# Performance work log

Hardware: AMD Instinct MI355X
Metric: run time of the kernel (lower is better)

## Reference

```python
import jax, jax.numpy as jnp
import numpy as np

D_MODEL = 1024
NUM_HEADS = 16
D_K = D_MODEL // NUM_HEADS
B, T = 2, 2048


def setup_inputs() -> dict:
    key = jax.random.key(0)
    ks = jax.random.split(key, 9)
    s = 1.0 / np.sqrt(D_MODEL)
    inp = {"x": jax.random.normal(ks[0], (B, T, D_MODEL), dtype=jnp.float32)}
    for i, name in enumerate(["q", "k", "v", "out"]):
        inp[f"W_{name}"] = jax.random.uniform(ks[1 + 2 * i], (D_MODEL, D_MODEL), jnp.float32, -s, s)
        inp[f"b_{name}"] = jax.random.uniform(ks[2 + 2 * i], (D_MODEL,), jnp.float32, -s, s)
    return inp


def reference(x, W_q, b_q, W_k, b_k, W_v, b_v, W_out, b_out):
    b, t, _ = x.shape
    # torch Linear: y = x @ W.T + b
    def proj(inp, W, bias):
        y = inp @ W.T + bias
        return y.reshape(b, -1, NUM_HEADS, D_K).transpose(0, 2, 1, 3)  # [B,H,T,d_k]

    Q = proj(x, W_q, b_q)
    K = proj(x, W_k, b_k)
    V = proj(x, W_v, b_v)
    scores = jnp.einsum("bhqd,bhkd->bhqk", Q, K) / jnp.sqrt(jnp.float32(D_K))
    attn = jax.nn.softmax(scores, axis=-1)
    ctx = jnp.einsum("bhqk,bhkd->bhqd", attn, V)
    ctx = ctx.transpose(0, 2, 1, 3).reshape(b, t, D_MODEL)
    return ctx @ W_out.T + b_out
```

## Files before the change

### kernel.cpp

```cpp
#include <hip/hip_runtime.h>
#include <hip/hip_bf16.h>

typedef __attribute__((ext_vector_type(8))) short short8;
typedef __attribute__((ext_vector_type(4))) short short4v;
typedef __attribute__((ext_vector_type(4))) float floatx4;

__device__ __forceinline__ unsigned short f2b(float f) {
  unsigned int v;
  __builtin_memcpy(&v, &f, 4);
  unsigned int r = (v + 0x7FFFu + ((v >> 16) & 1u)) >> 16;
  return (unsigned short)r;
}

__device__ __forceinline__ unsigned int f2b_pk(float a, float b) {
  unsigned int ua, ub;
  __builtin_memcpy(&ua, &a, 4);
  __builtin_memcpy(&ub, &b, 4);
  ua = ua + 0x7FFFu + ((ua >> 16) & 1u);
  ub = ub + 0x7FFFu + ((ub >> 16) & 1u);
#if __has_builtin(__builtin_amdgcn_perm)
  return __builtin_amdgcn_perm(ub, ua, 0x07060302u);
#else
  return (ub & 0xFFFF0000u) | (ua >> 16);
#endif
}

__device__ __forceinline__ float fast_exp2(float x) {
#if __has_builtin(__builtin_amdgcn_exp2f)
  return __builtin_amdgcn_exp2f(x);
#else
  return __builtin_exp2f(x);
#endif
}

__device__ __forceinline__ void async_copy16(const void* g, void* l) {
  __builtin_amdgcn_global_load_lds(
      (const __attribute__((address_space(1))) unsigned int*)g,
      (__attribute__((address_space(3))) unsigned int*)l, 16, 0, 0);
}

#define QSCALE 0.18033688011112042f

__global__ __launch_bounds__(256) void cvt_all_kernel(
    const float* __restrict__ x,
    const float* __restrict__ w0, const float* __restrict__ w1,
    const float* __restrict__ w2, const float* __restrict__ w3,
    unsigned short* __restrict__ xb,
    unsigned short* __restrict__ d0, unsigned short* __restrict__ d1,
    unsigned short* __restrict__ d2, unsigned short* __restrict__ d3)
{
  int gid = blockIdx.x * 256 + threadIdx.x;
  const float* src;
  unsigned short* dst;
  size_t off;
  if (gid < (1 << 20)) {
    src = x; dst = xb; off = gid;
  } else {
    int g = gid - (1 << 20);
    int w = g >> 18;
    off = g & 0x3FFFF;
    src = (w == 0) ? w0 : (w == 1) ? w1 : (w == 2) ? w2 : w3;
    dst = (w == 0) ? d0 : (w == 1) ? d1 : (w == 2) ? d2 : d3;
  }
  floatx4 v = *(const floatx4*)(src + off * 4);
  unsigned int lo = f2b_pk(v[0], v[1]), hi = f2b_pk(v[2], v[3]);
  unsigned long long r = ((unsigned long long)hi << 32) | lo;
  *(unsigned long long*)(dst + off * 4) = r;
}

__global__ __launch_bounds__(256) void gemm_qkv_kernel(
    const unsigned short* __restrict__ A,
    const unsigned short* __restrict__ W0, const unsigned short* __restrict__ W1,
    const unsigned short* __restrict__ W2,
    const float* __restrict__ bias0, const float* __restrict__ bias1,
    const float* __restrict__ bias2,
    unsigned short* __restrict__ Qo, unsigned short* __restrict__ Ko,
    unsigned short* __restrict__ VTo)
{
  const int z = blockIdx.z;
  const unsigned short* W  = (z == 0) ? W0 : (z == 1) ? W1 : W2;
  const float* bias        = (z == 0) ? bias0 : (z == 1) ? bias1 : bias2;

  __shared__ alignas(16) unsigned short sA[128 * 64];
  __shared__ alignas(16) unsigned short sB[128 * 64];

  const int tid  = threadIdx.x;
  const int lane = tid & 63;
  const int wave = tid >> 6;
  const int col  = lane & 15;
  const int quad = lane >> 4;
  const int wm   = (wave >> 1) * 64;
  const int wn   = (wave & 1) * 64;
  const int m0   = blockIdx.y * 128;
  const int n0   = blockIdx.x * 128;
  const int c7   = col & 7;

  floatx4 acc[4][4];
#pragma unroll
  for (int i = 0; i < 4; ++i)
#pragma unroll
    for (int j = 0; j < 4; ++j) acc[i][j] = (floatx4){0.f, 0.f, 0.f, 0.f};

  for (int k0 = 0; k0 < 1024; k0 += 64) {
    __syncthreads();
#pragma unroll
    for (int i = 0; i < 4; ++i) {
      int c   = i * 256 + tid;
      int row = c >> 3;
      int ko  = ((c & 7) ^ (row & 7)) * 8;
      async_copy16(A + (size_t)(m0 + row) * 1024 + k0 + ko, sA + c * 8);
      async_copy16(W + (size_t)(n0 + row) * 1024 + k0 + ko, sB + c * 8);
    }
    __syncthreads();
#pragma unroll
    for (int ks = 0; ks < 2; ++ks) {
      const int rp = ((ks * 4 + quad) ^ c7) * 8;
      short8 af[4], bf[4];
#pragma unroll
      for (int mi = 0; mi < 4; ++mi)
        af[mi] = *(const short8*)(sA + (wm + mi * 16 + col) * 64 + rp);
#pragma unroll
      for (int ni = 0; ni < 4; ++ni)
        bf[ni] = *(const short8*)(sB + (wn + ni * 16 + col) * 64 + rp);
#pragma unroll
      for (int mi = 0; mi < 4; ++mi)
#pragma unroll
        for (int ni = 0; ni < 4; ++ni)
          acc[mi][ni] = __builtin_amdgcn_mfma_f32_16x16x32_bf16(af[mi], bf[ni], acc[mi][ni], 0, 0, 0);
    }
  }

#pragma unroll
  for (int ni = 0; ni < 4; ++ni) {
    int n = n0 + wn + ni * 16 + col;
    float bv = bias[n];
#pragma unroll
    for (int mi = 0; mi < 4; ++mi) {
      int mbase = m0 + wm + mi * 16 + quad * 4;
      if (z == 2) {
        int d = n & 63, h = n >> 6;
        int bb = mbase >> 11, t = mbase & 2047;
        unsigned int lo = f2b_pk(acc[mi][ni][0] + bv, acc[mi][ni][1] + bv);
        unsigned int hi = f2b_pk(acc[mi][ni][2] + bv, acc[mi][ni][3] + bv);
        unsigned long long wv = ((unsigned long long)hi << 32) | lo;
        *(unsigned long long*)(VTo + (((size_t)bb * 16 + h) * 64 + d) * 2048 + t) = wv;
      } else {
#pragma unroll
        for (int r = 0; r < 4; ++r) {
          int m = mbase + r;
          float val = acc[mi][ni][r] + bv;
          if (z == 0) Qo[(size_t)m * 1024 + n] = f2b(val * QSCALE);
          else        Ko[(size_t)m * 1024 + n] = f2b(val);
        }
      }
    }
  }
}

__global__ __launch_bounds__(256) void gemm_out_kernel(
    const unsigned short* __restrict__ A, const unsigned short* __restrict__ W,
    const float* __restrict__ bias, float* __restrict__ DF)
{
  __shared__ alignas(16) unsigned short sA[128 * 64];
  __shared__ alignas(16) unsigned short sB[128 * 64];

  const int tid  = threadIdx.x;
  const int lane = tid & 63;
  const int wave = tid >> 6;
  const int col  = lane & 15;
  const int quad = lane >> 4;
  const int wm   = (wave >> 1) * 64;
  const int wn   = (wave & 1) * 64;
  const int m0   = blockIdx.y * 128;
  const int n0   = blockIdx.x * 128;
  const int c7   = col & 7;

  floatx4 acc[4][4];
#pragma unroll
  for (int i = 0; i < 4; ++i)
#pragma unroll
    for (int j = 0; j < 4; ++j) acc[i][j] = (floatx4){0.f, 0.f, 0.f, 0.f};

  for (int k0 = 0; k0 < 1024; k0 += 64) {
    __syncthreads();
#pragma unroll
    for (int i = 0; i < 4; ++i) {
      int c   = i * 256 + tid;
      int row = c >> 3;
      int ko  = ((c & 7) ^ (row & 7)) * 8;
      async_copy16(A + (size_t)(m0 + row) * 1024 + k0 + ko, sA + c * 8);
      async_copy16(W + (size_t)(n0 + row) * 1024 + k0 + ko, sB + c * 8);
    }
    __syncthreads();
#pragma unroll
    for (int ks = 0; ks < 2; ++ks) {
      const int rp = ((ks * 4 + quad) ^ c7) * 8;
      short8 af[4], bf[4];
#pragma unroll
      for (int mi = 0; mi < 4; ++mi)
        af[mi] = *(const short8*)(sA + (wm + mi * 16 + col) * 64 + rp);
#pragma unroll
      for (int ni = 0; ni < 4; ++ni)
        bf[ni] = *(const short8*)(sB + (wn + ni * 16 + col) * 64 + rp);
#pragma unroll
      for (int mi = 0; mi < 4; ++mi)
#pragma unroll
        for (int ni = 0; ni < 4; ++ni)
          acc[mi][ni] = __builtin_amdgcn_mfma_f32_16x16x32_bf16(af[mi], bf[ni], acc[mi][ni], 0, 0, 0);
    }
  }

#pragma unroll
  for (int ni = 0; ni < 4; ++ni) {
    int n = n0 + wn + ni * 16 + col;
    float bv = bias[n];
#pragma unroll
    for (int mi = 0; mi < 4; ++mi) {
      int mbase = m0 + wm + mi * 16 + quad * 4;
#pragma unroll
      for (int r = 0; r < 4; ++r)
        DF[(size_t)(mbase + r) * 1024 + n] = acc[mi][ni][r] + bv;
    }
  }
}

__global__ __launch_bounds__(256, 2) void attention_kernel(
    const unsigned short* __restrict__ Q, const unsigned short* __restrict__ K,
    const unsigned short* __restrict__ VT, unsigned short* __restrict__ CTX)
{
  __shared__ alignas(16) unsigned short sK[2][4096];
  __shared__ alignas(16) unsigned short sV[2][4096];
  __shared__ alignas(16) unsigned short sP[4][32 * 64];

  const int flat = blockIdx.x;
  const int idx  = flat >> 3;
  const int bh   = (flat & 7) * 4 + (idx >> 4);
  const int q0   = (idx & 15) * 128;
  const int b = bh >> 4, h = bh & 15;

  const int tid  = threadIdx.x;
  const int lane = tid & 63;
  const int wave = tid >> 6;
  const int col  = lane & 15;
  const int quad = lane >> 4;
  const int c7   = col & 7;
  const int swz8 = (quad ^ ((col >> 1) & 3)) * 8;

  const int srow = tid >> 2;
  const int sko  = ((tid & 3) ^ ((tid >> 3) & 3)) * 8;

  const unsigned short* kbase = K + ((size_t)b * 2048 + srow) * 1024 + h * 64;
  const unsigned short* vbase = VT + ((size_t)bh * 64 + srow) * 2048;

  short8 qfA[2], qfB[2];
  {
    const unsigned short* qp =
        Q + ((size_t)(b * 2048 + q0 + wave * 32 + col)) * 1024 + h * 64 + quad * 8;
    qfA[0] = *(const short8*)qp;
    qfA[1] = *(const short8*)(qp + 32);
    qfB[0] = *(const short8*)(qp + 16 * 1024);
    qfB[1] = *(const short8*)(qp + 16 * 1024 + 32);
  }

#pragma unroll
  for (int i = 0; i < 2; ++i) {
    async_copy16(kbase + i * 32 + sko, sK[0] + (i * 256 + tid) * 8);
    async_copy16(vbase + i * 32 + sko, sV[0] + (i * 256 + tid) * 8);
  }

  floatx4 OA[4], OB[4];
#pragma unroll
  for (int f = 0; f < 4; ++f) {
    OA[f] = (floatx4){0.f, 0.f, 0.f, 0.f};
    OB[f] = (floatx4){0.f, 0.f, 0.f, 0.f};
  }
  float laccA = 0.f, laccB = 0.f;

  unsigned short* myP = &sP[wave][0];

#pragma unroll 2
  for (int kt = 0; kt < 2048; kt += 64) {
    const int cur = (kt >> 6) & 1;
    const unsigned short* sKc = sK[cur];
    const unsigned short* sVc = sV[cur];
    __syncthreads();
    if (kt + 64 < 2048) {
      const int nxt = cur ^ 1;
#pragma unroll
      for (int i = 0; i < 2; ++i) {
        async_copy16(kbase + (size_t)(kt + 64) * 1024 + i * 32 + sko,
                     sK[nxt] + (i * 256 + tid) * 8);
        async_copy16(vbase + (kt + 64) + i * 32 + sko,
                     sV[nxt] + (i * 256 + tid) * 8);
      }
    }

    floatx4 STA[4], STB[4];
    __builtin_amdgcn_s_setprio(1);
#pragma unroll
    for (int f = 0; f < 4; ++f) {
      short8 kf0 = *(const short8*)(sKc + (f * 16 + col) * 32 + swz8);
      short8 kf1 = *(const short8*)(sKc + 2048 + (f * 16 + col) * 32 + swz8);
      STA[f] = (floatx4){0.f, 0.f, 0.f, 0.f};
      STA[f] = __builtin_amdgcn_mfma_f32_16x16x32_bf16(kf0, qfA[0], STA[f], 0, 0, 0);
      STA[f] = __builtin_amdgcn_mfma_f32_16x16x32_bf16(kf1, qfA[1], STA[f], 0, 0, 0);
      STB[f] = (floatx4){0.f, 0.f, 0.f, 0.f};
      STB[f] = __builtin_amdgcn_mfma_f32_16x16x32_bf16(kf0, qfB[0], STB[f], 0, 0, 0);
      STB[f] = __builtin_amdgcn_mfma_f32_16x16x32_bf16(kf1, qfB[1], STB[f], 0, 0, 0);
    }
    __builtin_amdgcn_s_setprio(0);

#pragma unroll
    for (int f = 0; f < 4; ++f) {
      float a0 = fast_exp2(STA[f][0]);
      float a1 = fast_exp2(STA[f][1]);
      float a2 = fast_exp2(STA[f][2]);
      float a3 = fast_exp2(STA[f][3]);
      laccA += (a0 + a1) + (a2 + a3);
      unsigned long long wA =
          ((unsigned long long)f2b_pk(a2, a3) << 32) | f2b_pk(a0, a1);
      *(unsigned long long*)(myP + col * 64 +
                             (((f * 2 + (quad >> 1)) ^ c7) * 8) + (quad & 1) * 4) = wA;
      float b0 = fast_exp2(STB[f][0]);
      float b1 = fast_exp2(STB[f][1]);
      float b2 = fast_exp2(STB[f][2]);
      float b3 = fast_exp2(STB[f][3]);
      laccB += (b0 + b1) + (b2 + b3);
      unsigned long long wB =
          ((unsigned long long)f2b_pk(b2, b3) << 32) | f2b_pk(b0, b1);
      *(unsigned long long*)(myP + (16 + col) * 64 +
                             (((f * 2 + (quad >> 1)) ^ c7) * 8) + (quad & 1) * 4) = wB;
    }

    short8 pfA0 = *(const short8*)(myP + col * 64 + ((quad ^ c7) * 8));
    short8 pfA1 = *(const short8*)(myP + col * 64 + (((quad + 4) ^ c7) * 8));
    short8 pfB0 = *(const short8*)(myP + (16 + col) * 64 + ((quad ^ c7) * 8));
    short8 pfB1 = *(const short8*)(myP + (16 + col) * 64 + (((quad + 4) ^ c7) * 8));
    __builtin_amdgcn_s_setprio(1);
#pragma unroll
    for (int f = 0; f < 4; ++f) {
      short8 vf0 = *(const short8*)(sVc + (f * 16 + col) * 32 + swz8);
      short8 vf1 = *(const short8*)(sVc + 2048 + (f * 16 + col) * 32 + swz8);
      OA[f] = __builtin_amdgcn_mfma_f32_16x16x32_bf16(pfA0, vf0, OA[f], 0, 0, 0);
      OA[f] = __builtin_amdgcn_mfma_f32_16x16x32_bf16(pfA1, vf1, OA[f], 0, 0, 0);
      OB[f] = __builtin_amdgcn_mfma_f32_16x16x32_bf16(pfB0, vf0, OB[f], 0, 0, 0);
      OB[f] = __builtin_amdgcn_mfma_f32_16x16x32_bf16(pfB1, vf1, OB[f], 0, 0, 0);
    }
    __builtin_amdgcn_s_setprio(0);
  }

  laccA += __shfl_xor(laccA, 16, 64);
  laccA += __shfl_xor(laccA, 32, 64);
  laccB += __shfl_xor(laccB, 16, 64);
  laccB += __shfl_xor(laccB, 32, 64);
  float invA[4], invB[4];
#pragma unroll
  for (int r = 0; r < 4; ++r) {
    invA[r] = 1.f / __shfl(laccA, quad * 4 + r, 16);
    invB[r] = 1.f / __shfl(laccB, quad * 4 + r, 16);
  }

#pragma unroll
  for (int f = 0; f < 4; ++f) {
#pragma unroll
    for (int r = 0; r < 4; ++r) {
      int qA = q0 + wave * 32 + quad * 4 + r;
      int d = f * 16 + col;
      CTX[(size_t)(b * 2048 + qA) * 1024 + h * 64 + d] = f2b(OA[f][r] * invA[r]);
      CTX[(size_t)(b * 2048 + qA + 16) * 1024 + h * 64 + d] = f2b(OB[f][r] * invB[r]);
    }
  }
}

extern "C" void kernel_launch(void* const* d_in, const int* in_sizes, int n_in,
                              void* d_out, int out_size, void* d_ws, size_t ws_size,
                              hipStream_t stream) {
  const float* x   = (const float*)d_in[0];
  const float* W_q = (const float*)d_in[1];
  const float* b_q = (const float*)d_in[2];
  const float* W_k = (const float*)d_in[3];
  const float* b_k = (const float*)d_in[4];
  const float* W_v = (const float*)d_in[5];
  const float* b_v = (const float*)d_in[6];
  const float* W_o = (const float*)d_in[7];
  const float* b_o = (const float*)d_in[8];
  float* out = (float*)d_out;

  const size_t NX = (size_t)4096 * 1024;
  const size_t NW = (size_t)1024 * 1024;

  unsigned short* p   = (unsigned short*)d_ws;
  unsigned short* xb  = p;  p += NX;
  unsigned short* Wqb = p;  p += NW;
  unsigned short* Wkb = p;  p += NW;
  unsigned short* Wvb = p;  p += NW;
  unsigned short* Wob = p;  p += NW;
  unsigned short* Q   = p;  p += NX;
  unsigned short* Kb  = p;  p += NX;
  unsigned short* VT  = p;  p += NX;
  unsigned short* CTX = p;  p += NX;

  dim3 blk(256);
  cvt_all_kernel<<<dim3(8192), blk, 0, stream>>>(
      x, W_q, W_k, W_v, W_o, xb, Wqb, Wkb, Wvb, Wob);
  gemm_qkv_kernel<<<dim3(8, 32, 3), blk, 0, stream>>>(
      xb, Wqb, Wkb, Wvb, b_q, b_k, b_v, Q, Kb, VT);
  attention_kernel<<<dim3(512), blk, 0, stream>>>(Q, Kb, VT, CTX);
  gemm_out_kernel<<<dim3(8, 32), blk, 0, stream>>>(CTX, Wob, b_o, out);
}
```

Baseline: 206.0 us.

## Halve GEMM K-tile to 32 and shrink output-projection N-tile to 64

Both projection GEMMs now stage 32-wide K slices in shared memory instead of 64, with a new 4-chunk XOR swizzle for bank-conflict avoidance. This halves LDS use per block, which may let more blocks share a CU. The output GEMM also moves from 128x128 to 128x64 tiles, doubling its grid to 512 blocks so the GPU's CUs are better filled. The cost is twice as many K iterations and barriers, and less register reuse per block in the output GEMM.

Result: faster. 190.8 us (median of 2 runs) (-7.4%).

```diff
diff --git a/kernel.cpp b/kernel.cpp
--- a/kernel.cpp
+++ b/kernel.cpp
@@ -81,8 +81,8 @@
   const unsigned short* W  = (z == 0) ? W0 : (z == 1) ? W1 : W2;
   const float* bias        = (z == 0) ? bias0 : (z == 1) ? bias1 : bias2;
 
-  __shared__ alignas(16) unsigned short sA[128 * 64];
-  __shared__ alignas(16) unsigned short sB[128 * 64];
+  __shared__ alignas(16) unsigned short sA[128 * 32];
+  __shared__ alignas(16) unsigned short sB[128 * 32];
 
   const int tid  = threadIdx.x;
   const int lane = tid & 63;
@@ -93,7 +93,7 @@
   const int wn   = (wave & 1) * 64;
   const int m0   = blockIdx.y * 128;
   const int n0   = blockIdx.x * 128;
-  const int c7   = col & 7;
+  const int swz8 = (quad ^ ((col >> 1) & 3)) * 8;
 
   floatx4 acc[4][4];
 #pragma unroll
@@ -101,33 +101,30 @@
 #pragma unroll
     for (int j = 0; j < 4; ++j) acc[i][j] = (floatx4){0.f, 0.f, 0.f, 0.f};
 
-  for (int k0 = 0; k0 < 1024; k0 += 64) {
+  for (int k0 = 0; k0 < 1024; k0 += 32) {
     __syncthreads();
 #pragma unroll
-    for (int i = 0; i < 4; ++i) {
+    for (int i = 0; i < 2; ++i) {
       int c   = i * 256 + tid;
-      int row = c >> 3;
-      int ko  = ((c & 7) ^ (row & 7)) * 8;
+      int row = c >> 2;
+      int cs  = (c & 3) ^ ((c >> 3) & 3);
+      int ko  = cs * 8;
       async_copy16(A + (size_t)(m0 + row) * 1024 + k0 + ko, sA + c * 8);
       async_copy16(W + (size_t)(n0 + row) * 1024 + k0 + ko, sB + c * 8);
     }
     __syncthreads();
-#pragma unroll
-    for (int ks = 0; ks < 2; ++ks) {
-      const int rp = ((ks * 4 + quad) ^ c7) * 8;
-      short8 af[4], bf[4];
-#pragma unroll
-      for (int mi = 0; mi < 4; ++mi)
-        af[mi] = *(const short8*)(sA + (wm + mi * 16 + col) * 64 + rp);
+    short8 af[4], bf[4];
+#pragma unroll
+    for (int mi = 0; mi < 4; ++mi)
+      af[mi] = *(const short8*)(sA + (wm + mi * 16 + col) * 32 + swz8);
+#pragma unroll
+    for (int ni = 0; ni < 4; ++ni)
+      bf[ni] = *(const short8*)(sB + (wn + ni * 16 + col) * 32 + swz8);
+#pragma unroll
+    for (int mi = 0; mi < 4; ++mi)
 #pragma unroll
       for (int ni = 0; ni < 4; ++ni)
-        bf[ni] = *(const short8*)(sB + (wn + ni * 16 + col) * 64 + rp);
-#pragma unroll
-      for (int mi = 0; mi < 4; ++mi)
-#pragma unroll
-        for (int ni = 0; ni < 4; ++ni)
-          acc[mi][ni] = __builtin_amdgcn_mfma_f32_16x16x32_bf16(af[mi], bf[ni], acc[mi][ni], 0, 0, 0);
-    }
+        acc[mi][ni] = __builtin_amdgcn_mfma_f32_16x16x32_bf16(af[mi], bf[ni], acc[mi][ni], 0, 0, 0);
   }
 
 #pragma unroll
@@ -161,8 +158,8 @@
     const unsigned short* __restrict__ A, const unsigned short* __restrict__ W,
     const float* __restrict__ bias, float* __restrict__ DF)
 {
-  __shared__ alignas(16) unsigned short sA[128 * 64];
-  __shared__ alignas(16) unsigned short sB[128 * 64];
+  __shared__ alignas(16) unsigned short sA[128 * 32];
+  __shared__ alignas(16) unsigned short sB[64 * 32];
 
   const int tid  = threadIdx.x;
   const int lane = tid & 63;
@@ -170,48 +167,48 @@
   const int col  = lane & 15;
   const int quad = lane >> 4;
   const int wm   = (wave >> 1) * 64;
-  const int wn   = (wave & 1) * 64;
+  const int wn   = (wave & 1) * 32;
   const int m0   = blockIdx.y * 128;
-  const int n0   = blockIdx.x * 128;
-  const int c7   = col & 7;
-
-  floatx4 acc[4][4];
+  const int n0   = blockIdx.x * 64;
+  const int swz8 = (quad ^ ((col >> 1) & 3)) * 8;
+
+  floatx4 acc[4][2];
 #pragma unroll
   for (int i = 0; i < 4; ++i)
 #pragma unroll
-    for (int j = 0; j < 4; ++j) acc[i][j] = (floatx4){0.f, 0.f, 0.f, 0.f};
-
-  for (int k0 = 0; k0 < 1024; k0 += 64) {
+    for (int j = 0; j < 2; ++j) acc[i][j] = (floatx4){0.f, 0.f, 0.f, 0.f};
+
+  for (int k0 = 0; k0 < 1024; k0 += 32) {
     __syncthreads();
 #pragma unroll
-    for (int i = 0; i < 4; ++i) {
+    for (int i = 0; i < 2; ++i) {
       int c   = i * 256 + tid;
-      int row = c >> 3;
-      int ko  = ((c & 7) ^ (row & 7)) * 8;
-      async_copy16(A + (size_t)(m0 + row) * 1024 + k0 + ko, sA + c * 8);
-      async_copy16(W + (size_t)(n0 + row) * 1024 + k0 + ko, sB + c * 8);
+      int row = c >> 2;
+      int cs  = (c & 3) ^ ((c >> 3) & 3);
+      async_copy16(A + (size_t)(m0 + row) * 1024 + k0 + cs * 8, sA + c * 8);
+    }
+    {
+      int row = tid >> 2;
+      int cs  = (tid & 3) ^ ((tid >> 3) & 3);
+      async_copy16(W + (size_t)(n0 + row) * 1024 + k0 + cs * 8, sB + tid * 8);
     }
     __syncthreads();
-#pragma unroll
-    for (int ks = 0; ks < 2; ++ks) {
-      const int rp = ((ks * 4 + quad) ^ c7) * 8;
-      short8 af[4], bf[4];
-#pragma unroll
-      for (int mi = 0; mi < 4; ++mi)
-        af[mi] = *(const short8*)(sA + (wm + mi * 16 + col) * 64 + rp);
-#pragma unroll
-      for (int ni = 0; ni < 4; ++ni)
-        bf[ni] = *(const short8*)(sB + (wn + ni * 16 + col) * 64 + rp);
-#pragma unroll
-      for (int mi = 0; mi < 4; ++mi)
-#pragma unroll
-        for (int ni = 0; ni < 4; ++ni)
-          acc[mi][ni] = __builtin_amdgcn_mfma_f32_16x16x32_bf16(af[mi], bf[ni], acc[mi][ni], 0, 0, 0);
-    }
-  }
-
-#pragma unroll
-  for (int ni = 0; ni < 4; ++ni) {
+    short8 af[4], bf[2];
+#pragma unroll
+    for (int mi = 0; mi < 4; ++mi)
+      af[mi] = *(const short8*)(sA + (wm + mi * 16 + col) * 32 + swz8);
+#pragma unroll
+    for (int ni = 0; ni < 2; ++ni)
+      bf[ni] = *(const short8*)(sB + (wn + ni * 16 + col) * 32 + swz8);
+#pragma unroll
+    for (int mi = 0; mi < 4; ++mi)
+#pragma unroll
+      for (int ni = 0; ni < 2; ++ni)
+        acc[mi][ni] = __builtin_amdgcn_mfma_f32_16x16x32_bf16(af[mi], bf[ni], acc[mi][ni], 0, 0, 0);
+  }
+
+#pragma unroll
+  for (int ni = 0; ni < 2; ++ni) {
     int n = n0 + wn + ni * 16 + col;
     float bv = bias[n];
 #pragma unroll
@@ -406,5 +403,5 @@
   gemm_qkv_kernel<<<dim3(8, 32, 3), blk, 0, stream>>>(
       xb, Wqb, Wkb, Wvb, b_q, b_k, b_v, Q, Kb, VT);
   attention_kernel<<<dim3(512), blk, 0, stream>>>(Q, Kb, VT, CTX);
-  gemm_out_kernel<<<dim3(8, 32), blk, 0, stream>>>(CTX, Wob, b_o, out);
-}
+  gemm_out_kernel<<<dim3(16, 32), blk, 0, stream>>>(CTX, Wob, b_o, out);
+}
```
